# Kernel tuning notes

Hardware: AMD Instinct MI355X
Metric: run time of the kernel (lower is better)

## Reference

```python
import jax, jax.numpy as jnp
import numpy as np

N_SRC, N_DST, E = 10000, 10000, 640000
S, T, O, H = 128, 128, 128, 4
D = O // H


def setup_inputs() -> dict:
    key = jax.random.key(0)
    ks = jax.random.split(key, 12)
    f = lambda k, shape, fan: jax.random.normal(k, shape, dtype=jnp.float32) / np.float32(np.sqrt(fan))
    return {
        "x_src": jax.random.normal(ks[0], (N_SRC, S), dtype=jnp.float32),
        "x_dst": jax.random.normal(ks[1], (N_DST, T), dtype=jnp.float32),
        "W_pred1": f(ks[2], (S, T), T),
        "b_pred1": jnp.zeros((S,), jnp.float32),
        "W_pred2": f(ks[3], (S, S), S),
        "b_pred2": jnp.zeros((S,), jnp.float32),
        "W_res": f(ks[4], (H * D, S), S),
        "W_src": f(ks[5], (H * D, S), S),
        "W_dst": f(ks[6], (H * D, T), T),
        "att_src": jax.random.normal(ks[7], (1, H, D), dtype=jnp.float32) * 0.01,
        "att_dst": jax.random.normal(ks[8], (1, H, D), dtype=jnp.float32) * 0.01,
        "W_self": f(ks[9], (H * D, T), T),
        "b_self": jnp.zeros((H * D,), jnp.float32),
        "edge_src": jax.random.randint(ks[10], (E,), 0, N_SRC),
        "edge_dst": jax.random.randint(ks[11], (E,), 0, N_DST),
        "num_dst": N_DST,
    }


def reference(x_src, x_dst, W_pred1, b_pred1, W_pred2, b_pred2, W_res, W_src, W_dst,
              att_src, att_dst, W_self, b_self, edge_src, edge_dst, num_dst):
    h, d = att_src.shape[1], att_src.shape[2]
    # residual prediction path: pred_mlp(x_dst) = Lin2(ReLU(Lin1(x_dst)))
    pred = jax.nn.relu(x_dst @ W_pred1.T + b_pred1) @ W_pred2.T + b_pred2  # [Ndst,S]
    residual = x_src[edge_src] - pred[edge_dst]                            # [E,S]
    # per-node attention logits (equivalent to gather-then-dot, cheaper)
    a_s = ((x_src @ W_src.T).reshape(-1, h, d) * att_src).sum(-1)          # [Nsrc,H]
    a_d = ((x_dst @ W_dst.T).reshape(-1, h, d) * att_dst).sum(-1)          # [Ndst,H]
    alpha = jax.nn.leaky_relu(a_s[edge_src] + a_d[edge_dst], 0.2)          # [E,H]
    # edge softmax over incoming edges of each destination node
    amax = jax.ops.segment_max(alpha, edge_dst, num_segments=num_dst)      # [Ndst,H]
    ex = jnp.exp(alpha - amax[edge_dst])
    denom = jax.ops.segment_sum(ex, edge_dst, num_segments=num_dst)
    alpha = ex / (denom[edge_dst] + 1e-16)                                 # [E,H]
    # attention-weighted aggregation of transformed residuals
    msg = (residual @ W_res.T).reshape(-1, h, d) * alpha[:, :, None]       # [E,H,D]
    agg = jax.ops.segment_sum(msg.reshape(-1, h * d), edge_dst, num_segments=num_dst)
    return agg + x_dst @ W_self.T + b_self                                 # [Ndst,H*D]
```

## Files before the change

### kernel.cpp

```cpp
#include <hip/hip_runtime.h>

#define LEAKY 0.2f
#define CAP 160
#define CAPB 8192
#define CHUNK 6144

#define FMA4(A, S, V) do { (A).x += (S)*(V).x; (A).y += (S)*(V).y; (A).z += (S)*(V).z; (A).w += (S)*(V).w; } while (0)

struct GemmJob { const float* X; const float* W; const float* B; float* Y; int M; int relu; };

__device__ __forceinline__ void gemm128_block(
    const float* __restrict__ X, const float* __restrict__ W,
    const float* __restrict__ B, float* __restrict__ Y,
    int M, int relu, int row0,
    float* __restrict__ XsT , float* __restrict__ WTs ) {
  if (row0 >= M) return;
  const int tid = threadIdx.x;
  const int tx = tid & 15;
  const int ty = tid >> 4;
  float4 acc[8][2];
#pragma unroll
  for (int i = 0; i < 8; i++) {
    acc[i][0] = make_float4(0.f, 0.f, 0.f, 0.f);
    acc[i][1] = make_float4(0.f, 0.f, 0.f, 0.f);
  }
  const int rS = tid >> 1;
  const int kb = (tid & 1) * 16;

  for (int k0 = 0; k0 < 128; k0 += 32) {
    int rr = row0 + rS; if (rr >= M) rr = M - 1;
    const float* xp = X + (size_t)rr * 128 + k0 + kb;
    float4 a0 = *(const float4*)xp;
    float4 a1 = *(const float4*)(xp + 4);
    float4 a2 = *(const float4*)(xp + 8);
    float4 a3 = *(const float4*)(xp + 12);
    XsT[(kb + 0) * 128 + rS] = a0.x; XsT[(kb + 1) * 128 + rS] = a0.y;
    XsT[(kb + 2) * 128 + rS] = a0.z; XsT[(kb + 3) * 128 + rS] = a0.w;
    XsT[(kb + 4) * 128 + rS] = a1.x; XsT[(kb + 5) * 128 + rS] = a1.y;
    XsT[(kb + 6) * 128 + rS] = a1.z; XsT[(kb + 7) * 128 + rS] = a1.w;
    XsT[(kb + 8) * 128 + rS] = a2.x; XsT[(kb + 9) * 128 + rS] = a2.y;
    XsT[(kb +10) * 128 + rS] = a2.z; XsT[(kb +11) * 128 + rS] = a2.w;
    XsT[(kb +12) * 128 + rS] = a3.x; XsT[(kb +13) * 128 + rS] = a3.y;
    XsT[(kb +14) * 128 + rS] = a3.z; XsT[(kb +15) * 128 + rS] = a3.w;

    const float* wp = W + (size_t)rS * 128 + k0 + kb;
    float4 b0 = *(const float4*)wp;
    float4 b1 = *(const float4*)(wp + 4);
    float4 b2 = *(const float4*)(wp + 8);
    float4 b3 = *(const float4*)(wp + 12);
    WTs[(kb + 0) * 128 + rS] = b0.x; WTs[(kb + 1) * 128 + rS] = b0.y;
    WTs[(kb + 2) * 128 + rS] = b0.z; WTs[(kb + 3) * 128 + rS] = b0.w;
    WTs[(kb + 4) * 128 + rS] = b1.x; WTs[(kb + 5) * 128 + rS] = b1.y;
    WTs[(kb + 6) * 128 + rS] = b1.z; WTs[(kb + 7) * 128 + rS] = b1.w;
    WTs[(kb + 8) * 128 + rS] = b2.x; WTs[(kb + 9) * 128 + rS] = b2.y;
    WTs[(kb +10) * 128 + rS] = b2.z; WTs[(kb +11) * 128 + rS] = b2.w;
    WTs[(kb +12) * 128 + rS] = b3.x; WTs[(kb +13) * 128 + rS] = b3.y;
    WTs[(kb +14) * 128 + rS] = b3.z; WTs[(kb +15) * 128 + rS] = b3.w;
    __syncthreads();

#pragma unroll
    for (int k = 0; k < 32; k++) {
      float4 xa = *(const float4*)&XsT[k * 128 + ty * 4];
      float4 xb = *(const float4*)&XsT[k * 128 + 64 + ty * 4];
      float4 w0 = *(const float4*)&WTs[k * 128 + tx * 4];
      float4 w1 = *(const float4*)&WTs[k * 128 + 64 + tx * 4];
      FMA4(acc[0][0], xa.x, w0); FMA4(acc[0][1], xa.x, w1);
      FMA4(acc[1][0], xa.y, w0); FMA4(acc[1][1], xa.y, w1);
      FMA4(acc[2][0], xa.z, w0); FMA4(acc[2][1], xa.z, w1);
      FMA4(acc[3][0], xa.w, w0); FMA4(acc[3][1], xa.w, w1);
      FMA4(acc[4][0], xb.x, w0); FMA4(acc[4][1], xb.x, w1);
      FMA4(acc[5][0], xb.y, w0); FMA4(acc[5][1], xb.y, w1);
      FMA4(acc[6][0], xb.z, w0); FMA4(acc[6][1], xb.z, w1);
      FMA4(acc[7][0], xb.w, w0); FMA4(acc[7][1], xb.w, w1);
    }
    __syncthreads();
  }

  float4 bv0 = make_float4(0.f, 0.f, 0.f, 0.f);
  float4 bv1 = make_float4(0.f, 0.f, 0.f, 0.f);
  if (B) { bv0 = *(const float4*)(B + tx * 4); bv1 = *(const float4*)(B + 64 + tx * 4); }
#pragma unroll
  for (int i = 0; i < 8; i++) {
    int r = row0 + (i < 4 ? ty * 4 + i : 64 + ty * 4 + (i - 4));
    if (r < M) {
      float4 o0, o1;
      o0.x = acc[i][0].x + bv0.x; o0.y = acc[i][0].y + bv0.y;
      o0.z = acc[i][0].z + bv0.z; o0.w = acc[i][0].w + bv0.w;
      o1.x = acc[i][1].x + bv1.x; o1.y = acc[i][1].y + bv1.y;
      o1.z = acc[i][1].z + bv1.z; o1.w = acc[i][1].w + bv1.w;
      if (relu) {
        o0.x = fmaxf(o0.x, 0.f); o0.y = fmaxf(o0.y, 0.f);
        o0.z = fmaxf(o0.z, 0.f); o0.w = fmaxf(o0.w, 0.f);
        o1.x = fmaxf(o1.x, 0.f); o1.y = fmaxf(o1.y, 0.f);
        o1.z = fmaxf(o1.z, 0.f); o1.w = fmaxf(o1.w, 0.f);
      }
      *(float4*)(Y + (size_t)r * 128 + tx * 4) = o0;
      *(float4*)(Y + (size_t)r * 128 + 64 + tx * 4) = o1;
    }
  }
}

__device__ __forceinline__ void attn32_block(const float* __restrict__ X,
                                             const float* __restrict__ v,
                                             float* __restrict__ a, int M, int blk,
                                             float* __restrict__ vsf ) {
  int tid = threadIdx.x;
  for (int i = tid; i < 512; i += 256) vsf[i + ((i >> 5) << 2)] = v[i];
  __syncthreads();
  int g = tid >> 3, l = tid & 7;
  int n = blk * 32 + g;
  if (n >= M) return;
  const float* xp = X + (size_t)n * 128 + l * 16;
  float4 x0 = *(const float4*)xp;
  float4 x1 = *(const float4*)(xp + 4);
  float4 x2 = *(const float4*)(xp + 8);
  float4 x3 = *(const float4*)(xp + 12);
  const float4* vv = (const float4*)vsf;
  int s = l * 18;
  float4 p = make_float4(0.f, 0.f, 0.f, 0.f);
  FMA4(p, x0.x, vv[s + 0]); FMA4(p, x0.y, vv[s + 1]); FMA4(p, x0.z, vv[s + 2]); FMA4(p, x0.w, vv[s + 3]);
  FMA4(p, x1.x, vv[s + 4]); FMA4(p, x1.y, vv[s + 5]); FMA4(p, x1.z, vv[s + 6]); FMA4(p, x1.w, vv[s + 7]);
  FMA4(p, x2.x, vv[s + 9]); FMA4(p, x2.y, vv[s +10]); FMA4(p, x2.z, vv[s +11]); FMA4(p, x2.w, vv[s +12]);
  FMA4(p, x3.x, vv[s +13]); FMA4(p, x3.y, vv[s +14]); FMA4(p, x3.z, vv[s +15]); FMA4(p, x3.w, vv[s +16]);
#pragma unroll
  for (int off = 1; off < 8; off <<= 1) {
    p.x += __shfl_xor(p.x, off, 64);
    p.y += __shfl_xor(p.y, off, 64);
    p.z += __shfl_xor(p.z, off, 64);
    p.w += __shfl_xor(p.w, off, 64);
  }
  if (l == 0) *(float4*)(a + (size_t)n * 4) = p;
}

__global__ __launch_bounds__(256) void phase1(
    const float* __restrict__ Wsrc, const float* __restrict__ attsrc,
    const float* __restrict__ Wdst, const float* __restrict__ attdst,
    const float* __restrict__ W_res, const float* __restrict__ W2,
    const float* __restrict__ b2,
    float* __restrict__ v_src, float* __restrict__ v_dst,
    float* __restrict__ Wc, float* __restrict__ bc,
    const int* __restrict__ edge_src, const int* __restrict__ edge_dst,
    int* __restrict__ gcnt, int* __restrict__ bin, int E, int Nd, int NB) {
  __shared__ int pk[CHUNK];
  __shared__ int hist[160];
  __shared__ int gbaseArr[160];
  __shared__ int lcur[160];
  int bx = blockIdx.x, tid = threadIdx.x;
  if (bx == 0) {
    int which = tid >> 7, k = tid & 127;
    const float* W = which ? Wdst : Wsrc;
    const float* att = which ? attdst : attsrc;
    float* v = which ? v_dst : v_src;
    float s[4] = {0.f, 0.f, 0.f, 0.f};
#pragma unroll
    for (int h = 0; h < 4; h++)
      for (int d = 0; d < 32; d++)
        s[h] += W[(size_t)(h * 32 + d) * 128 + k] * att[h * 32 + d];
#pragma unroll
    for (int h = 0; h < 4; h++) v[k * 4 + h] = s[h];
  } else if (bx == 1) {
    if (tid < 128) {
      float s = 0.f;
      for (int i = 0; i < 128; i++) s += W_res[(size_t)tid * 128 + i] * b2[i];
      bc[tid] = s;
    }
  } else if (bx < 66) {
    int id = (bx - 2) * 256 + tid;
    int o = id >> 7, j = id & 127;
    float s = 0.f;
    for (int i = 0; i < 128; i++) s += W_res[(size_t)o * 128 + i] * W2[(size_t)i * 128 + j];
    Wc[(size_t)o * 128 + j] = s;
  } else {
    int chunk = bx - 66;
    int e0 = chunk * CHUNK;
    int n = E - e0; if (n > CHUNK) n = CHUNK;
    if (n <= 0) return;
    for (int i = tid; i < NB; i += 256) hist[i] = 0;
    __syncthreads();
    for (int i = tid; i < n; i += 256) {
      int s = edge_src[e0 + i], d = edge_dst[e0 + i];
      pk[i] = (s << 14) | d;
      atomicAdd(&hist[d >> 6], 1);
    }
    __syncthreads();
    for (int b = tid; b < NB; b += 256) {
      gbaseArr[b] = atomicAdd(&gcnt[b], hist[b]);
      lcur[b] = 0;
    }
    __syncthreads();
    for (int i = tid; i < n; i += 256) {
      int p = pk[i];
      int b = (p & 16383) >> 6;
      int off = gbaseArr[b] + atomicAdd(&lcur[b], 1);
      if (off < CAPB) bin[(size_t)b * CAPB + off] = p;
    }
  }
}

__global__ __launch_bounds__(256) void phase2(
    GemmJob j0, GemmJob j1, GemmJob j2, GemmJob ju,
    const float* __restrict__ x_src, const float* __restrict__ x_dst,
    const float* __restrict__ v_src, const float* __restrict__ v_dst,
    float* __restrict__ a_s, float* __restrict__ a_d,
    const int* __restrict__ gcnt, const int* __restrict__ bin,
    int* __restrict__ sorted_src, int* __restrict__ rstart, int* __restrict__ rend,
    int* __restrict__ done_relu, int Ns, int Nd, int NB,
    int G, int As, int Ad) {
  __shared__ float smem[8192];
  int bx = blockIdx.x, tid = threadIdx.x;
  if (bx < 3 * G) {
    GemmJob J = (bx < G) ? j0 : (bx < 2 * G) ? j1 : j2;
    gemm128_block(J.X, J.W, J.B, J.Y, J.M, J.relu, (bx % G) * 128, smem, smem + 4096);
    if (bx < G) {
      __syncthreads();
      if (tid == 0) __hip_atomic_fetch_add(done_relu, 1, __ATOMIC_RELEASE, __HIP_MEMORY_SCOPE_AGENT);
    }
  } else if (bx < 3 * G + As) {
    attn32_block(x_src, v_src, a_s, Ns, bx - 3 * G, smem);
  } else if (bx < 3 * G + As + Ad) {
    attn32_block(x_dst, v_dst, a_d, Nd, bx - 3 * G - As, smem);
  } else if (bx < 3 * G + As + Ad + NB) {
    int b = bx - (3 * G + As + Ad);
    int* hist2  = (int*)smem;
    int* starts = (int*)smem + 64;
    int* lcur2  = (int*)smem + 128;
    int cnt = gcnt[b]; if (cnt > CAPB) cnt = CAPB;
    size_t base = (size_t)b * CAPB;
    if (tid < 64) hist2[tid] = 0;
    __syncthreads();
    for (int i = tid; i < cnt; i += 256) atomicAdd(&hist2[bin[base + i] & 63], 1);
    __syncthreads();
    if (tid < 64) {
      int v = hist2[tid];
      int incl = v;
#pragma unroll
      for (int off = 1; off < 64; off <<= 1) {
        int t = __shfl_up(incl, off, 64);
        if (tid >= off) incl += t;
      }
      int st = incl - v;
      starts[tid] = st;
      lcur2[tid] = st;
      int dst = (b << 6) + tid;
      if (dst < Nd) {
        rstart[dst] = (int)base + st;
        rend[dst]   = (int)base + st + v;
      }
    }
    __syncthreads();
    for (int i = tid; i < cnt; i += 256) {
      int p = bin[base + i];
      int j = p & 63;
      int lp = atomicAdd(&lcur2[j], 1);
      sorted_src[base + lp] = p >> 14;
    }
  } else {
    if (tid == 0) {
      while (__hip_atomic_load(done_relu, __ATOMIC_ACQUIRE, __HIP_MEMORY_SCOPE_AGENT) < G)
        __builtin_amdgcn_s_sleep(2);
    }
    __syncthreads();
    int bb = bx - (3 * G + As + Ad + NB);
    gemm128_block(ju.X, ju.W, ju.B, ju.Y, ju.M, ju.relu, bb * 128, smem, smem + 4096);
  }
}

__global__ __launch_bounds__(128) void agg_kernel(
    const int* __restrict__ rstart, const int* __restrict__ rend,
    const int* __restrict__ sorted_src,
    const float* __restrict__ a_s, const float* __restrict__ a_d,
    const float* __restrict__ u_src, const float* __restrict__ u_pred,
    const float* __restrict__ self_o, float* __restrict__ out) {
  int dst = blockIdx.x, tid = threadIdx.x;
  __shared__ float wbuf[CAP * 4];
  __shared__ int srcbuf[CAP];
  __shared__ float4 red4[2];
  __shared__ float4 redv[32];
  __shared__ float inv_s[4], sA_s[4];
  int start = rstart[dst];
  int deg = rend[dst] - start;
  float4 ad4 = *(const float4*)(a_d + (size_t)dst * 4);
  float s0 = 0.f, s1 = 0.f, s2 = 0.f, s3 = 0.f;
  for (int i = tid; i < deg; i += 128) {
    int src = sorted_src[start + i];
    float4 as4 = *(const float4*)(a_s + (size_t)src * 4);
    float l0 = as4.x + ad4.x; l0 = l0 > 0.f ? l0 : LEAKY * l0;
    float l1 = as4.y + ad4.y; l1 = l1 > 0.f ? l1 : LEAKY * l1;
    float l2 = as4.z + ad4.z; l2 = l2 > 0.f ? l2 : LEAKY * l2;
    float l3 = as4.w + ad4.w; l3 = l3 > 0.f ? l3 : LEAKY * l3;
    float w0 = __expf(l0), w1 = __expf(l1), w2 = __expf(l2), w3 = __expf(l3);
    if (i < CAP) {
      wbuf[i * 4 + 0] = w0; wbuf[i * 4 + 1] = w1;
      wbuf[i * 4 + 2] = w2; wbuf[i * 4 + 3] = w3;
      srcbuf[i] = src;
    }
    s0 += w0; s1 += w1; s2 += w2; s3 += w3;
  }
  int lane = tid & 63, wv = tid >> 6;
#pragma unroll
  for (int off = 32; off > 0; off >>= 1) {
    s0 += __shfl_xor(s0, off, 64);
    s1 += __shfl_xor(s1, off, 64);
    s2 += __shfl_xor(s2, off, 64);
    s3 += __shfl_xor(s3, off, 64);
  }
  if (lane == 0) red4[wv] = make_float4(s0, s1, s2, s3);
  __syncthreads();
  if (tid == 0) {
    float dx = red4[0].x + red4[1].x;
    float dy = red4[0].y + red4[1].y;
    float dz = red4[0].z + red4[1].z;
    float dw = red4[0].w + red4[1].w;
    inv_s[0] = 1.f / (dx + 1e-16f); sA_s[0] = dx * inv_s[0];
    inv_s[1] = 1.f / (dy + 1e-16f); sA_s[1] = dy * inv_s[1];
    inv_s[2] = 1.f / (dz + 1e-16f); sA_s[2] = dz * inv_s[2];
    inv_s[3] = 1.f / (dw + 1e-16f); sA_s[3] = dw * inv_s[3];
  }
  __syncthreads();

  int c4 = tid & 31, rgrp = tid >> 5, h = c4 >> 3;
  int coff = c4 * 4;
  float4 acc0 = make_float4(0.f,0.f,0.f,0.f), acc1 = acc0, acc2 = acc0, acc3 = acc0;
  int cap = deg < CAP ? deg : CAP;
  int i = rgrp;
  for (; i + 12 < cap; i += 16) {
    int sA = srcbuf[i], sB = srcbuf[i + 4], sC = srcbuf[i + 8], sD = srcbuf[i + 12];
    float wA = wbuf[i * 4 + h], wB = wbuf[(i + 4) * 4 + h];
    float wC = wbuf[(i + 8) * 4 + h], wD = wbuf[(i + 12) * 4 + h];
    float4 uA = *(const float4*)(u_src + (size_t)sA * 128 + coff);
    float4 uB = *(const float4*)(u_src + (size_t)sB * 128 + coff);
    float4 uC = *(const float4*)(u_src + (size_t)sC * 128 + coff);
    float4 uD = *(const float4*)(u_src + (size_t)sD * 128 + coff);
    FMA4(acc0, wA, uA); FMA4(acc1, wB, uB); FMA4(acc2, wC, uC); FMA4(acc3, wD, uD);
  }
  for (; i < cap; i += 4) {
    int s_ = srcbuf[i];
    float w = wbuf[i * 4 + h];
    float4 u = *(const float4*)(u_src + (size_t)s_ * 128 + coff);
    FMA4(acc0, w, u);
  }
  if (deg > CAP) {
    float adh = (h == 0) ? ad4.x : (h == 1) ? ad4.y : (h == 2) ? ad4.z : ad4.w;
    for (int k = CAP + rgrp; k < deg; k += 4) {
      int src = sorted_src[start + k];
      float l = a_s[(size_t)src * 4 + h] + adh;
      l = l > 0.f ? l : LEAKY * l;
      float w = __expf(l);
      float4 u = *(const float4*)(u_src + (size_t)src * 128 + coff);
      FMA4(acc0, w, u);
    }
  }
  float4 acc;
  acc.x = acc0.x + acc1.x + acc2.x + acc3.x;
  acc.y = acc0.y + acc1.y + acc2.y + acc3.y;
  acc.z = acc0.z + acc1.z + acc2.z + acc3.z;
  acc.w = acc0.w + acc1.w + acc2.w + acc3.w;
  acc.x += __shfl_xor(acc.x, 32, 64);
  acc.y += __shfl_xor(acc.y, 32, 64);
  acc.z += __shfl_xor(acc.z, 32, 64);
  acc.w += __shfl_xor(acc.w, 32, 64);
  if (tid >= 64 && tid < 96) redv[c4] = acc;
  __syncthreads();
  if (tid < 32) {
    float4 r = redv[c4];
    acc.x += r.x; acc.y += r.y; acc.z += r.z; acc.w += r.w;
    float4 up = *(const float4*)(u_pred + (size_t)dst * 128 + coff);
    float4 so = *(const float4*)(self_o + (size_t)dst * 128 + coff);
    float iv = inv_s[h], sa = sA_s[h];
    float4 o;
    o.x = acc.x * iv - sa * up.x + so.x;
    o.y = acc.y * iv - sa * up.y + so.y;
    o.z = acc.z * iv - sa * up.z + so.z;
    o.w = acc.w * iv - sa * up.w + so.w;
    *(float4*)(out + (size_t)dst * 128 + coff) = o;
  }
}

extern "C" void kernel_launch(void* const* d_in, const int* in_sizes, int n_in,
                              void* d_out, int out_size, void* d_ws, size_t ws_size,
                              hipStream_t stream) {
  const float* x_src   = (const float*)d_in[0];
  const float* x_dst   = (const float*)d_in[1];
  const float* W_pred1 = (const float*)d_in[2];
  const float* b_pred1 = (const float*)d_in[3];
  const float* W_pred2 = (const float*)d_in[4];
  const float* b_pred2 = (const float*)d_in[5];
  const float* W_res   = (const float*)d_in[6];
  const float* W_src   = (const float*)d_in[7];
  const float* W_dst   = (const float*)d_in[8];
  const float* att_src = (const float*)d_in[9];
  const float* att_dst = (const float*)d_in[10];
  const float* W_self  = (const float*)d_in[11];
  const float* b_self  = (const float*)d_in[12];
  const int* edge_src  = (const int*)d_in[13];
  const int* edge_dst  = (const int*)d_in[14];
  int Ns = in_sizes[0] / 128;
  int Nd = in_sizes[1] / 128;
  int E  = in_sizes[13];
  float* out = (float*)d_out;
  int NB = (Nd + 63) >> 6;

  char* ws = (char*)d_ws;
  auto alloc = [&](size_t bytes) -> char* {
    char* p = ws;
    ws += (bytes + 255) & ~(size_t)255;
    return p;
  };
  float* relu1  = (float*)alloc((size_t)Nd * 128 * 4);
  float* u_src  = (float*)alloc((size_t)Ns * 128 * 4);
  float* u_pred = (float*)alloc((size_t)Nd * 128 * 4);
  float* self_o = (float*)alloc((size_t)Nd * 128 * 4);
  float* a_s    = (float*)alloc((size_t)Ns * 4 * 4);
  float* a_d    = (float*)alloc((size_t)Nd * 4 * 4);
  float* v_src  = (float*)alloc(128 * 4 * 4);
  float* v_dst  = (float*)alloc(128 * 4 * 4);
  float* Wc     = (float*)alloc(128 * 128 * 4);
  float* bc     = (float*)alloc(128 * 4);
  int* gcnt     = (int*)alloc((size_t)(NB + 1) * 4);
  int* done_relu = gcnt + NB;
  int* rstart   = (int*)alloc((size_t)Nd * 4);
  int* rend     = (int*)alloc((size_t)Nd * 4);
  int* bin      = (int*)alloc((size_t)NB * CAPB * 4);
  int* sorted_src = (int*)alloc((size_t)NB * CAPB * 4);

  hipMemsetAsync(gcnt, 0, (size_t)(NB + 1) * sizeof(int), stream);

  int NCH = (E + CHUNK - 1) / CHUNK;
  hipLaunchKernelGGL(phase1, dim3(66 + NCH), dim3(256), 0, stream,
                     W_src, att_src, W_dst, att_dst, W_res, W_pred2, b_pred2,
                     v_src, v_dst, Wc, bc, edge_src, edge_dst, gcnt, bin, E, Nd, NB);

  int maxM = Ns > Nd ? Ns : Nd;
  int G  = (maxM + 127) / 128;
  int As = (Ns + 31) / 32;
  int Ad = (Nd + 31) / 32;
  GemmJob jA{ x_dst, W_pred1, b_pred1, relu1, Nd, 1 };
  GemmJob jB{ x_src, W_res,   nullptr, u_src, Ns, 0 };
  GemmJob jC{ x_dst, W_self,  b_self,  self_o, Nd, 0 };
  GemmJob jU{ relu1, Wc,      bc,      u_pred, Nd, 0 };
  int GU = (Nd + 127) / 128;
  hipLaunchKernelGGL(phase2, dim3(3 * G + As + Ad + NB + GU), dim3(256), 0, stream,
                     jA, jB, jC, jU, x_src, x_dst, v_src, v_dst, a_s, a_d,
                     gcnt, bin, sorted_src, rstart, rend, done_relu,
                     Ns, Nd, NB, G, As, Ad);

  hipLaunchKernelGGL(agg_kernel, dim3(Nd), dim3(128), 0, stream,
                     rstart, rend, sorted_src, a_s, a_d, u_src, u_pred, self_o, out);
}
```

Before: 196.0 us.

## Move relu GEMM into phase1, interleave block roles, pair destinations per agg block

Computes the first pred-MLP GEMM inside phase1 so phase2 no longer needs a spin-waiting dependent GEMM with an atomic flag. Both phase kernels remap block indices with a strided permutation so heterogeneous work types are spread across CUs. The edge binning chunk is shrunk to create more, smaller blocks, and bin counter atomics are skipped for empty bins. The aggregation kernel processes two destination nodes per 256-thread block to reduce block count and launch overhead. The trade-off is more global atomics from the extra chunks, and phase1 becomes heavier.

```diff
diff --git a/kernel.cpp b/kernel.cpp
--- a/kernel.cpp
+++ b/kernel.cpp
@@ -3,7 +3,7 @@
 #define LEAKY 0.2f
 #define CAP 160
 #define CAPB 8192
-#define CHUNK 6144
+#define CHUNK 2048
 
 #define FMA4(A, S, V) do { (A).x += (S)*(V).x; (A).y += (S)*(V).y; (A).z += (S)*(V).z; (A).w += (S)*(V).w; } while (0)
 
@@ -137,16 +137,17 @@
     const float* __restrict__ Wdst, const float* __restrict__ attdst,
     const float* __restrict__ W_res, const float* __restrict__ W2,
     const float* __restrict__ b2,
+    GemmJob jA,
     float* __restrict__ v_src, float* __restrict__ v_dst,
     float* __restrict__ Wc, float* __restrict__ bc,
     const int* __restrict__ edge_src, const int* __restrict__ edge_dst,
-    int* __restrict__ gcnt, int* __restrict__ bin, int E, int Nd, int NB) {
-  __shared__ int pk[CHUNK];
-  __shared__ int hist[160];
-  __shared__ int gbaseArr[160];
-  __shared__ int lcur[160];
+    int* __restrict__ gcnt, int* __restrict__ bin,
+    int E, int Nd, int NB, int GA, int Q1, int T1) {
+  __shared__ float smem[8192];
   int bx = blockIdx.x, tid = threadIdx.x;
-  if (bx == 0) {
+  int u = (bx & 7) * Q1 + (bx >> 3);
+  if (u >= T1) return;
+  if (u == 0) {
     int which = tid >> 7, k = tid & 127;
     const float* W = which ? Wdst : Wsrc;
     const float* att = which ? attdst : attsrc;
@@ -158,21 +159,26 @@
         s[h] += W[(size_t)(h * 32 + d) * 128 + k] * att[h * 32 + d];
 #pragma unroll
     for (int h = 0; h < 4; h++) v[k * 4 + h] = s[h];
-  } else if (bx == 1) {
+  } else if (u == 1) {
     if (tid < 128) {
       float s = 0.f;
       for (int i = 0; i < 128; i++) s += W_res[(size_t)tid * 128 + i] * b2[i];
       bc[tid] = s;
     }
-  } else if (bx < 66) {
-    int id = (bx - 2) * 256 + tid;
+  } else if (u < 66) {
+    int id = (u - 2) * 256 + tid;
     int o = id >> 7, j = id & 127;
     float s = 0.f;
     for (int i = 0; i < 128; i++) s += W_res[(size_t)o * 128 + i] * W2[(size_t)i * 128 + j];
     Wc[(size_t)o * 128 + j] = s;
+  } else if (u < 66 + GA) {
+    gemm128_block(jA.X, jA.W, jA.B, jA.Y, jA.M, jA.relu, (u - 66) * 128, smem, smem + 4096);
   } else {
-    int chunk = bx - 66;
-    int e0 = chunk * CHUNK;
+    int* pk    = (int*)smem;
+    int* hist  = (int*)smem + CHUNK;
+    int* gbase = hist + 160;
+    int* lcur  = gbase + 160;
+    int e0 = (u - 66 - GA) * CHUNK;
     int n = E - e0; if (n > CHUNK) n = CHUNK;
     if (n <= 0) return;
     for (int i = tid; i < NB; i += 256) hist[i] = 0;
@@ -184,46 +190,42 @@
     }
     __syncthreads();
     for (int b = tid; b < NB; b += 256) {
-      gbaseArr[b] = atomicAdd(&gcnt[b], hist[b]);
+      gbase[b] = hist[b] ? atomicAdd(&gcnt[b], hist[b]) : 0;
       lcur[b] = 0;
     }
     __syncthreads();
     for (int i = tid; i < n; i += 256) {
       int p = pk[i];
       int b = (p & 16383) >> 6;
-      int off = gbaseArr[b] + atomicAdd(&lcur[b], 1);
+      int off = gbase[b] + atomicAdd(&lcur[b], 1);
       if (off < CAPB) bin[(size_t)b * CAPB + off] = p;
     }
   }
 }
 
 __global__ __launch_bounds__(256) void phase2(
-    GemmJob j0, GemmJob j1, GemmJob j2, GemmJob ju,
+    GemmJob j0, GemmJob j1, GemmJob j2,
     const float* __restrict__ x_src, const float* __restrict__ x_dst,
     const float* __restrict__ v_src, const float* __restrict__ v_dst,
     float* __restrict__ a_s, float* __restrict__ a_d,
     const int* __restrict__ gcnt, const int* __restrict__ bin,
     int* __restrict__ sorted_src, int* __restrict__ rstart, int* __restrict__ rend,
-    int* __restrict__ done_relu, int Ns, int Nd, int NB,
-    int G, int As, int Ad) {
+    int Ns, int Nd, int NB, int G, int As, int Ad, int Q2, int T2) {
   __shared__ float smem[8192];
   int bx = blockIdx.x, tid = threadIdx.x;
-  if (bx < 3 * G) {
-    GemmJob J = (bx < G) ? j0 : (bx < 2 * G) ? j1 : j2;
-    gemm128_block(J.X, J.W, J.B, J.Y, J.M, J.relu, (bx % G) * 128, smem, smem + 4096);
-    if (bx < G) {
-      __syncthreads();
-      if (tid == 0) __hip_atomic_fetch_add(done_relu, 1, __ATOMIC_RELEASE, __HIP_MEMORY_SCOPE_AGENT);
-    }
-  } else if (bx < 3 * G + As) {
-    attn32_block(x_src, v_src, a_s, Ns, bx - 3 * G, smem);
-  } else if (bx < 3 * G + As + Ad) {
-    attn32_block(x_dst, v_dst, a_d, Nd, bx - 3 * G - As, smem);
-  } else if (bx < 3 * G + As + Ad + NB) {
-    int b = bx - (3 * G + As + Ad);
-    int* hist2  = (int*)smem;
-    int* starts = (int*)smem + 64;
-    int* lcur2  = (int*)smem + 128;
+  int u = (bx % 6) * Q2 + bx / 6;
+  if (u >= T2) return;
+  if (u < 3 * G) {
+    GemmJob J = (u < G) ? j0 : (u < 2 * G) ? j1 : j2;
+    gemm128_block(J.X, J.W, J.B, J.Y, J.M, J.relu, (u % G) * 128, smem, smem + 4096);
+  } else if (u < 3 * G + As) {
+    attn32_block(x_src, v_src, a_s, Ns, u - 3 * G, smem);
+  } else if (u < 3 * G + As + Ad) {
+    attn32_block(x_dst, v_dst, a_d, Nd, u - 3 * G - As, smem);
+  } else {
+    int b = u - (3 * G + As + Ad);
+    int* hist2 = (int*)smem;
+    int* lcur2 = (int*)smem + 64;
     int cnt = gcnt[b]; if (cnt > CAPB) cnt = CAPB;
     size_t base = (size_t)b * CAPB;
     if (tid < 64) hist2[tid] = 0;
@@ -239,7 +241,6 @@
         if (tid >= off) incl += t;
       }
       int st = incl - v;
-      starts[tid] = st;
       lcur2[tid] = st;
       int dst = (b << 6) + tid;
       if (dst < Nd) {
@@ -254,34 +255,34 @@
       int lp = atomicAdd(&lcur2[j], 1);
       sorted_src[base + lp] = p >> 14;
     }
-  } else {
-    if (tid == 0) {
-      while (__hip_atomic_load(done_relu, __ATOMIC_ACQUIRE, __HIP_MEMORY_SCOPE_AGENT) < G)
-        __builtin_amdgcn_s_sleep(2);
-    }
-    __syncthreads();
-    int bb = bx - (3 * G + As + Ad + NB);
-    gemm128_block(ju.X, ju.W, ju.B, ju.Y, ju.M, ju.relu, bb * 128, smem, smem + 4096);
-  }
-}
-
-__global__ __launch_bounds__(128) void agg_kernel(
+  }
+}
+
+__global__ __launch_bounds__(256) void phase3(
     const int* __restrict__ rstart, const int* __restrict__ rend,
     const int* __restrict__ sorted_src,
     const float* __restrict__ a_s, const float* __restrict__ a_d,
     const float* __restrict__ u_src, const float* __restrict__ u_pred,
-    const float* __restrict__ self_o, float* __restrict__ out) {
-  int dst = blockIdx.x, tid = threadIdx.x;
-  __shared__ float wbuf[CAP * 4];
-  __shared__ int srcbuf[CAP];
-  __shared__ float4 red4[2];
-  __shared__ float4 redv[32];
-  __shared__ float inv_s[4], sA_s[4];
+    const float* __restrict__ self_o, float* __restrict__ out, int Nd) {
+  __shared__ float smem[1920];
+  int bx = blockIdx.x, tid = threadIdx.x;
+  int half = tid >> 7;
+  int t = tid & 127;
+  int dst = bx * 2 + half;
+  if (dst >= Nd) return;
+
+  float* wbuf  = smem + half * 640;
+  int* srcbuf  = (int*)(smem + 1280) + half * 160;
+  float4* red4 = (float4*)(smem + 1600);
+  float4* redv = (float4*)(smem + 1616) + half * 32;
+  float* inv_s = smem + 1872 + half * 4;
+  float* sA_s  = smem + 1880 + half * 4;
+
   int start = rstart[dst];
   int deg = rend[dst] - start;
   float4 ad4 = *(const float4*)(a_d + (size_t)dst * 4);
   float s0 = 0.f, s1 = 0.f, s2 = 0.f, s3 = 0.f;
-  for (int i = tid; i < deg; i += 128) {
+  for (int i = t; i < deg; i += 128) {
     int src = sorted_src[start + i];
     float4 as4 = *(const float4*)(a_s + (size_t)src * 4);
     float l0 = as4.x + ad4.x; l0 = l0 > 0.f ? l0 : LEAKY * l0;
@@ -296,7 +297,7 @@
     }
     s0 += w0; s1 += w1; s2 += w2; s3 += w3;
   }
-  int lane = tid & 63, wv = tid >> 6;
+  int wave = tid >> 6;
 #pragma unroll
   for (int off = 32; off > 0; off >>= 1) {
     s0 += __shfl_xor(s0, off, 64);
@@ -304,13 +305,11 @@
     s2 += __shfl_xor(s2, off, 64);
     s3 += __shfl_xor(s3, off, 64);
   }
-  if (lane == 0) red4[wv] = make_float4(s0, s1, s2, s3);
+  if ((tid & 63) == 0) red4[wave] = make_float4(s0, s1, s2, s3);
   __syncthreads();
-  if (tid == 0) {
-    float dx = red4[0].x + red4[1].x;
-    float dy = red4[0].y + red4[1].y;
-    float dz = red4[0].z + red4[1].z;
-    float dw = red4[0].w + red4[1].w;
+  if (t == 0) {
+    float4 A = red4[half * 2], B = red4[half * 2 + 1];
+    float dx = A.x + B.x, dy = A.y + B.y, dz = A.z + B.z, dw = A.w + B.w;
     inv_s[0] = 1.f / (dx + 1e-16f); sA_s[0] = dx * inv_s[0];
     inv_s[1] = 1.f / (dy + 1e-16f); sA_s[1] = dy * inv_s[1];
     inv_s[2] = 1.f / (dz + 1e-16f); sA_s[2] = dz * inv_s[2];
@@ -318,7 +317,7 @@
   }
   __syncthreads();
 
-  int c4 = tid & 31, rgrp = tid >> 5, h = c4 >> 3;
+  int c4 = t & 31, rgrp = t >> 5, h = c4 >> 3;
   int coff = c4 * 4;
   float4 acc0 = make_float4(0.f,0.f,0.f,0.f), acc1 = acc0, acc2 = acc0, acc3 = acc0;
   int cap = deg < CAP ? deg : CAP;
@@ -336,8 +335,8 @@
   for (; i < cap; i += 4) {
     int s_ = srcbuf[i];
     float w = wbuf[i * 4 + h];
-    float4 u = *(const float4*)(u_src + (size_t)s_ * 128 + coff);
-    FMA4(acc0, w, u);
+    float4 uu = *(const float4*)(u_src + (size_t)s_ * 128 + coff);
+    FMA4(acc0, w, uu);
   }
   if (deg > CAP) {
     float adh = (h == 0) ? ad4.x : (h == 1) ? ad4.y : (h == 2) ? ad4.z : ad4.w;
@@ -346,8 +345,8 @@
       float l = a_s[(size_t)src * 4 + h] + adh;
       l = l > 0.f ? l : LEAKY * l;
       float w = __expf(l);
-      float4 u = *(const float4*)(u_src + (size_t)src * 128 + coff);
-      FMA4(acc0, w, u);
+      float4 uu = *(const float4*)(u_src + (size_t)src * 128 + coff);
+      FMA4(acc0, w, uu);
     }
   }
   float4 acc;
@@ -359,9 +358,9 @@
   acc.y += __shfl_xor(acc.y, 32, 64);
   acc.z += __shfl_xor(acc.z, 32, 64);
   acc.w += __shfl_xor(acc.w, 32, 64);
-  if (tid >= 64 && tid < 96) redv[c4] = acc;
+  if (t >= 64 && t < 96) redv[c4] = acc;
   __syncthreads();
-  if (tid < 32) {
+  if (t < 32) {
     float4 r = redv[c4];
     acc.x += r.x; acc.y += r.y; acc.z += r.z; acc.w += r.w;
     float4 up = *(const float4*)(u_pred + (size_t)dst * 128 + coff);
@@ -416,34 +415,38 @@
   float* v_dst  = (float*)alloc(128 * 4 * 4);
   float* Wc     = (float*)alloc(128 * 128 * 4);
   float* bc     = (float*)alloc(128 * 4);
-  int* gcnt     = (int*)alloc((size_t)(NB + 1) * 4);
-  int* done_relu = gcnt + NB;
+  int* gcnt     = (int*)alloc((size_t)NB * 4);
   int* rstart   = (int*)alloc((size_t)Nd * 4);
   int* rend     = (int*)alloc((size_t)Nd * 4);
   int* bin      = (int*)alloc((size_t)NB * CAPB * 4);
   int* sorted_src = (int*)alloc((size_t)NB * CAPB * 4);
 
-  hipMemsetAsync(gcnt, 0, (size_t)(NB + 1) * sizeof(int), stream);
-
+  hipMemsetAsync(gcnt, 0, (size_t)NB * sizeof(int), stream);
+
+  int GA  = (Nd + 127) / 128;
   int NCH = (E + CHUNK - 1) / CHUNK;
-  hipLaunchKernelGGL(phase1, dim3(66 + NCH), dim3(256), 0, stream,
-                     W_src, att_src, W_dst, att_dst, W_res, W_pred2, b_pred2,
-                     v_src, v_dst, Wc, bc, edge_src, edge_dst, gcnt, bin, E, Nd, NB);
+  int T1 = 66 + GA + NCH;
+  int Q1 = (T1 + 7) / 8;
+  GemmJob jA{ x_dst, W_pred1, b_pred1, relu1, Nd, 1 };
+  hipLaunchKernelGGL(phase1, dim3(Q1 * 8), dim3(256), 0, stream,
+                     W_src, att_src, W_dst, att_dst, W_res, W_pred2, b_pred2, jA,
+                     v_src, v_dst, Wc, bc, edge_src, edge_dst, gcnt, bin,
+                     E, Nd, NB, GA, Q1, T1);
 
   int maxM = Ns > Nd ? Ns : Nd;
   int G  = (maxM + 127) / 128;
   int As = (Ns + 31) / 32;
   int Ad = (Nd + 31) / 32;
-  GemmJob jA{ x_dst, W_pred1, b_pred1, relu1, Nd, 1 };
-  GemmJob jB{ x_src, W_res,   nullptr, u_src, Ns, 0 };
-  GemmJob jC{ x_dst, W_self,  b_self,  self_o, Nd, 0 };
-  GemmJob jU{ relu1, Wc,      bc,      u_pred, Nd, 0 };
-  int GU = (Nd + 127) / 128;
-  hipLaunchKernelGGL(phase2, dim3(3 * G + As + Ad + NB + GU), dim3(256), 0, stream,
-                     jA, jB, jC, jU, x_src, x_dst, v_src, v_dst, a_s, a_d,
-                     gcnt, bin, sorted_src, rstart, rend, done_relu,
-                     Ns, Nd, NB, G, As, Ad);
-
-  hipLaunchKernelGGL(agg_kernel, dim3(Nd), dim3(128), 0, stream,
-                     rstart, rend, sorted_src, a_s, a_d, u_src, u_pred, self_o, out);
-}
+  int T2 = 3 * G + As + Ad + NB;
+  int Q2 = (T2 + 5) / 6;
+  GemmJob jB{ x_src, W_res,  nullptr, u_src,  Ns, 0 };
+  GemmJob jC{ x_dst, W_self, b_self,  self_o, Nd, 0 };
+  GemmJob jU{ relu1, Wc,     bc,      u_pred, Nd, 0 };
+  hipLaunchKernelGGL(phase2, dim3(Q2 * 6), dim3(256), 0, stream,
+                     jB, jC, jU, x_src, x_dst, v_src, v_dst, a_s, a_d,
+                     gcnt, bin, sorted_src, rstart, rend,
+                     Ns, Nd, NB, G, As, Ad, Q2, T2);
+
+  hipLaunchKernelGGL(phase3, dim3((Nd + 1) / 2), dim3(256), 0, stream,
+                     rstart, rend, sorted_src, a_s, a_d, u_src, u_pred, self_o, out, Nd);
+}
```

Result: faster. 173.2 us (-11.6%).
